# Kernel tuning notes

Hardware: AMD Instinct MI355X
Metric: run time of the kernel (lower is better)

## Reference

```python
import jax, jax.numpy as jnp
import numpy as np

HIDDEN = 2048
N_HEADS = 32
N_KV_HEADS = 8
HEAD_DIM = HIDDEN // N_HEADS  # 64
KV_GROUPS = N_HEADS // N_KV_HEADS  # 4
ROPE_THETA = 10000.0
BSZ, SEQ = 2, 2048


def setup_inputs() -> dict:
    key = jax.random.key(0)
    ks = jax.random.split(key, 5)
    s = 0.02
    hidden_states = jax.random.normal(ks[0], (BSZ, SEQ, HIDDEN), jnp.float32)
    position_ids = jnp.broadcast_to(jnp.arange(SEQ, dtype=jnp.int32), (BSZ, SEQ))
    Wq = jax.random.normal(ks[1], (HIDDEN, HIDDEN), jnp.float32) * s
    Wk = jax.random.normal(ks[2], (N_KV_HEADS * HEAD_DIM, HIDDEN), jnp.float32) * s
    Wv = jax.random.normal(ks[3], (N_KV_HEADS * HEAD_DIM, HIDDEN), jnp.float32) * s
    Wo = jax.random.normal(ks[4], (HIDDEN, HIDDEN), jnp.float32) * s
    return {"hidden_states": hidden_states, "position_ids": position_ids,
            "Wq": Wq, "Wk": Wk, "Wv": Wv, "Wo": Wo}


def _rope_cos_sin(position_ids):
    # Llama rotary embedding: inv_freq over even dims, emb = [freqs, freqs]
    inv_freq = 1.0 / (ROPE_THETA ** (jnp.arange(0, HEAD_DIM, 2, dtype=jnp.float32) / HEAD_DIM))  # [Hd/2]
    freqs = position_ids.astype(jnp.float32)[..., None] * inv_freq  # [B, S, Hd/2]
    emb = jnp.concatenate([freqs, freqs], axis=-1)  # [B, S, Hd]
    return jnp.cos(emb), jnp.sin(emb)


def _rotate_half(x):
    x1, x2 = jnp.split(x, 2, axis=-1)
    return jnp.concatenate([-x2, x1], axis=-1)


def reference(hidden_states, position_ids, Wq, Wk, Wv, Wo):
    bsz, seq_len, _ = hidden_states.shape
    # projections (nn.Linear: y = x @ W.T)
    q = (hidden_states @ Wq.T).reshape(bsz, seq_len, N_HEADS, HEAD_DIM).transpose(0, 2, 1, 3)
    k = (hidden_states @ Wk.T).reshape(bsz, seq_len, N_KV_HEADS, HEAD_DIM).transpose(0, 2, 1, 3)
    v = (hidden_states @ Wv.T).reshape(bsz, seq_len, N_KV_HEADS, HEAD_DIM).transpose(0, 2, 1, 3)
    cos, sin = _rope_cos_sin(position_ids)  # [B, S, Hd]
    cos = cos[:, None, :, :]
    sin = sin[:, None, :, :]
    q = q * cos + _rotate_half(q) * sin
    k = k * cos + _rotate_half(k) * sin
    # GQA expand kv heads to full head count
    k = jnp.repeat(k, KV_GROUPS, axis=1)  # [B, H, S, Hd]
    v = jnp.repeat(v, KV_GROUPS, axis=1)
    # naive full-softmax attention (no causal mask, matching the source)
    scores = jnp.einsum('bhqd,bhkd->bhqk', q, k) / jnp.sqrt(jnp.float32(HEAD_DIM))
    attn_w = jax.nn.softmax(scores, axis=-1)
    attn_o = jnp.einsum('bhqk,bhkd->bhqd', attn_w, v)
    attn_o = attn_o.transpose(0, 2, 1, 3).reshape(bsz, seq_len, HIDDEN)
    return attn_o @ Wo.T
```

## Files before the change

kernel.cpp:

```cpp
#include <hip/hip_runtime.h>
#include <hip/hip_bf16.h>
#include <stdint.h>

#define HID 2048
#define NH 32
#define NKV 8
#define HD 64
#define BSZ 2
#define SEQ 2048
#define NROWS (BSZ*SEQ)
#define KVCOLS (NKV*HD)
#define QKVN 3072

typedef __attribute__((ext_vector_type(8))) short bf16x8;
typedef __attribute__((ext_vector_type(4))) float f32x4;
typedef __attribute__((ext_vector_type(16))) float f32x16;
typedef __attribute__((ext_vector_type(2))) unsigned int u32x2;

__device__ __forceinline__ unsigned short f2bf(float f) {
  union { float f; uint32_t u; } v; v.f = f;
  uint32_t r = v.u + 0x7FFFu + ((v.u >> 16) & 1u);
  return (unsigned short)(r >> 16);
}

__device__ __forceinline__ unsigned pack_bf16(float a, float b) {
  union { __hip_bfloat162 h; unsigned u; } cv;
  cv.h = __float22bfloat162_rn(make_float2(a, b));
  return cv.u;
}

__device__ __forceinline__ float sum16(const f32x16& s) {
  float a0 = s[0] + s[1], a1 = s[2] + s[3], a2 = s[4] + s[5], a3 = s[6] + s[7];
  float a4 = s[8] + s[9], a5 = s[10] + s[11], a6 = s[12] + s[13], a7 = s[14] + s[15];
  float b0 = a0 + a1, b1 = a2 + a3, b2 = a4 + a5, b3 = a6 + a7;
  return (b0 + b1) + (b2 + b3);
}

#define MKPB(S, B0) ({ \
  unsigned A_ = pack_bf16((S)[B0], (S)[(B0)+1]); \
  unsigned C_ = pack_bf16((S)[(B0)+2], (S)[(B0)+3]); \
  unsigned B_ = pack_bf16((S)[(B0)+4], (S)[(B0)+5]); \
  unsigned D_ = pack_bf16((S)[(B0)+6], (S)[(B0)+7]); \
  u32x2 r0_ = __builtin_amdgcn_permlane32_swap(A_, B_, false, false); \
  u32x2 r1_ = __builtin_amdgcn_permlane32_swap(C_, D_, false, false); \
  union { uint4 u; bf16x8 v; } cv_; \
  cv_.u.x = r0_.x; cv_.u.y = r1_.x; cv_.u.z = r0_.y; cv_.u.w = r1_.y; \
  cv_.v; })

#define ROPE_C (-0.41524101186092029f)
#define QSCL 0.18033688011112042f

#define C0 2097152
#define C1 3145728
#define C2 3407872
#define C3 3670016
#define CT 4718592
__global__ __launch_bounds__(256) void cvt_all(
    const float* __restrict__ hs, const float* __restrict__ wq,
    const float* __restrict__ wk, const float* __restrict__ wv,
    const float* __restrict__ wo,
    unsigned short* __restrict__ xb, unsigned short* __restrict__ wqkv,
    unsigned short* __restrict__ wob) {
  int i4 = blockIdx.x * 256 + threadIdx.x;
  const int stride = gridDim.x * 256;
  for (; i4 < CT; i4 += stride) {
    const float* src; unsigned short* dst;
    if (i4 < C0)      { src = hs + (size_t)i4 * 4;            dst = xb   + (size_t)i4 * 4; }
    else if (i4 < C1) { src = wq + (size_t)(i4 - C0) * 4;     dst = wqkv + (size_t)(i4 - C0) * 4; }
    else if (i4 < C2) { src = wk + (size_t)(i4 - C1) * 4;     dst = wqkv + 4194304 + (size_t)(i4 - C1) * 4; }
    else if (i4 < C3) { src = wv + (size_t)(i4 - C2) * 4;     dst = wqkv + 5242880 + (size_t)(i4 - C2) * 4; }
    else              { src = wo + (size_t)(i4 - C3) * 4;     dst = wob  + (size_t)(i4 - C3) * 4; }
    float4 v = *(const float4*)src;
    ushort4 o;
    o.x = f2bf(v.x); o.y = f2bf(v.y); o.z = f2bf(v.z); o.w = f2bf(v.w);
    *(ushort4*)dst = o;
  }
}

#define BM 128
#define BN 128
#define BK 32

__global__ __launch_bounds__(256) void gemm_btn(
    const unsigned short* __restrict__ A,
    const unsigned short* __restrict__ B,
    float* __restrict__ C,
    int M, int N, int K)
{
  __shared__ unsigned short As[2][BM * BK];
  __shared__ unsigned short Bs[2][BN * BK];
  const int t = threadIdx.x;
  const int w = t >> 6, l = t & 63;
  const int wr = w >> 1, wc = w & 1;

  const int nwg = gridDim.x * gridDim.y;
  const int lin = blockIdx.y * gridDim.x + blockIdx.x;
  const int swz = (lin & 7) * (nwg >> 3) + (lin >> 3);
  const int bx = swz % gridDim.x, by = swz / gridDim.x;

  const int row0 = by * BM, col0 = bx * BN;
  const int lr = l & 15, lk = (l >> 4) * 8;

  f32x4 acc[4][4];
  for (int i = 0; i < 4; ++i)
    for (int j = 0; j < 4; ++j)
      acc[i][j] = (f32x4){0.f, 0.f, 0.f, 0.f};

  auto stage = [&](int bi, int k0) {
    #pragma unroll
    for (int i = 0; i < 2; ++i) {
      int ebase = i * 2048 + w * 512;
      int e = ebase + l * 8;
      const unsigned short* srcA = A + (size_t)(row0 + (e >> 5)) * K + k0 + (e & 31);
      const unsigned short* srcB = B + (size_t)(col0 + (e >> 5)) * K + k0 + (e & 31);
      __builtin_amdgcn_global_load_lds((const __attribute__((address_space(1))) void*)srcA,
          (__attribute__((address_space(3))) void*)&As[bi][ebase], 16, 0, 0);
      __builtin_amdgcn_global_load_lds((const __attribute__((address_space(1))) void*)srcB,
          (__attribute__((address_space(3))) void*)&Bs[bi][ebase], 16, 0, 0);
    }
  };

  stage(0, 0);
  __syncthreads();
  int bi = 0;
  for (int k0 = 0; k0 < K; k0 += BK) {
    if (k0 + BK < K) stage(bi ^ 1, k0 + BK);
    bf16x8 a[4], b[4];
    #pragma unroll
    for (int mi = 0; mi < 4; ++mi)
      a[mi] = *(const bf16x8*)&As[bi][(wr * 64 + mi * 16 + lr) * BK + lk];
    #pragma unroll
    for (int ni = 0; ni < 4; ++ni)
      b[ni] = *(const bf16x8*)&Bs[bi][(wc * 64 + ni * 16 + lr) * BK + lk];
    #pragma unroll
    for (int mi = 0; mi < 4; ++mi)
      #pragma unroll
      for (int ni = 0; ni < 4; ++ni)
        acc[mi][ni] = __builtin_amdgcn_mfma_f32_16x16x32_bf16(a[mi], b[ni], acc[mi][ni], 0, 0, 0);
    __syncthreads();
    bi ^= 1;
  }

  const int crow = (l >> 4) * 4, ccol = l & 15;
  #pragma unroll
  for (int mi = 0; mi < 4; ++mi)
    #pragma unroll
    for (int ni = 0; ni < 4; ++ni) {
      float* cp = C + (size_t)(row0 + wr * 64 + mi * 16 + crow) * N + col0 + wc * 64 + ni * 16 + ccol;
      #pragma unroll
      for (int r = 0; r < 4; ++r)
        cp[(size_t)r * N] = acc[mi][ni][r];
    }
}

__global__ __launch_bounds__(256) void gemm_qkv(
    const unsigned short* __restrict__ A,
    const unsigned short* __restrict__ B,
    const int* __restrict__ pos_ids,
    unsigned short* __restrict__ Qb,
    unsigned short* __restrict__ Kb,
    unsigned short* __restrict__ Vt)
{
  __shared__ unsigned short Sh[4 * BM * BK];
  unsigned short* As = Sh;
  unsigned short* Bs = Sh + 2 * BM * BK;
  const int t = threadIdx.x;
  const int w = t >> 6, l = t & 63;
  const int wr = w >> 1, wc = w & 1;

  const int nwg = gridDim.x * gridDim.y;
  const int lin = blockIdx.y * gridDim.x + blockIdx.x;
  const int swz = (lin & 7) * (nwg >> 3) + (lin >> 3);
  const int bx = swz % gridDim.x, by = swz / gridDim.x;

  const int row0 = by * BM, col0 = bx * BN;
  const int lr = l & 15, lk = (l >> 4) * 8;

  f32x4 acc[4][4];
  for (int i = 0; i < 4; ++i)
    for (int j = 0; j < 4; ++j)
      acc[i][j] = (f32x4){0.f, 0.f, 0.f, 0.f};

  auto stage = [&](int bi, int k0) {
    #pragma unroll
    for (int i = 0; i < 2; ++i) {
      int ebase = i * 2048 + w * 512;
      int e = ebase + l * 8;
      const unsigned short* srcA = A + (size_t)(row0 + (e >> 5)) * HID + k0 + (e & 31);
      const unsigned short* srcB = B + (size_t)(col0 + (e >> 5)) * HID + k0 + (e & 31);
      __builtin_amdgcn_global_load_lds((const __attribute__((address_space(1))) void*)srcA,
          (__attribute__((address_space(3))) void*)&As[bi * BM * BK + ebase], 16, 0, 0);
      __builtin_amdgcn_global_load_lds((const __attribute__((address_space(1))) void*)srcB,
          (__attribute__((address_space(3))) void*)&Bs[bi * BN * BK + ebase], 16, 0, 0);
    }
  };

  stage(0, 0);
  __syncthreads();
  int bi = 0;
  for (int k0 = 0; k0 < HID; k0 += BK) {
    if (k0 + BK < HID) stage(bi ^ 1, k0 + BK);
    bf16x8 a[4], b[4];
    #pragma unroll
    for (int mi = 0; mi < 4; ++mi)
      a[mi] = *(const bf16x8*)&As[bi * BM * BK + (wr * 64 + mi * 16 + lr) * BK + lk];
    #pragma unroll
    for (int ni = 0; ni < 4; ++ni)
      b[ni] = *(const bf16x8*)&Bs[bi * BN * BK + (wc * 64 + ni * 16 + lr) * BK + lk];
    #pragma unroll
    for (int mi = 0; mi < 4; ++mi)
      #pragma unroll
      for (int ni = 0; ni < 4; ++ni)
        acc[mi][ni] = __builtin_amdgcn_mfma_f32_16x16x32_bf16(a[mi], b[ni], acc[mi][ni], 0, 0, 0);
    __syncthreads();
    bi ^= 1;
  }

  const int crow = (l >> 4) * 4, ccol = l & 15;
  const int colbase = col0 + wc * 64;
  const int b = row0 >> 11;

  if (colbase < HID + KVCOLS) {
    const bool isQ = colbase < HID;
    const float scl = isQ ? QSCL : 1.0f;
    const int hh = (isQ ? colbase : colbase - HID) >> 6;
    unsigned short* base = (isQ ? Qb + ((size_t)(b * NH + hh) * SEQ) * HD
                                : Kb + ((size_t)(b * NKV + hh) * SEQ) * HD);
    const float invf0 = exp2f((float)ccol * ROPE_C);
    const float invf1 = exp2f((float)(ccol + 16) * ROPE_C);
    #pragma unroll
    for (int mi = 0; mi < 4; ++mi) {
      const int rowb = row0 + wr * 64 + mi * 16 + crow;
      #pragma unroll
      for (int r = 0; r < 4; ++r) {
        const int row = rowb + r;
        const int s = row & (SEQ - 1);
        const float pos = (float)pos_ids[row];
        #pragma unroll
        for (int ni = 0; ni < 2; ++ni) {
          float sn, cs;
          __sincosf(pos * (ni ? invf1 : invf0), &sn, &cs);
          const float x1 = acc[mi][ni][r], x2 = acc[mi][ni + 2][r];
          unsigned short* p = base + (size_t)s * HD + ni * 16 + ccol;
          p[0]  = f2bf((x1 * cs - x2 * sn) * scl);
          p[32] = f2bf((x2 * cs + x1 * sn) * scl);
        }
      }
    }
  } else {
    const int cv = colbase - (HID + KVCOLS);
    const int kh = cv >> 6;
    unsigned short* vbase = Vt + ((size_t)(b * NKV + kh) * HD) * SEQ;
    const int s0row = (row0 + wr * 64) & (SEQ - 1);
    char* Tw = (char*)Sh + w * 8192;
    #pragma unroll
    for (int ni = 0; ni < 4; ++ni) {
      const int d = ni * 16 + ccol;
      #pragma unroll
      for (int mi = 0; mi < 4; ++mi) {
        const int sl = mi * 16 + crow;
        ushort4 o;
        o.x = f2bf(acc[mi][ni][0]);
        o.y = f2bf(acc[mi][ni][1]);
        o.z = f2bf(acc[mi][ni][2]);
        o.w = f2bf(acc[mi][ni][3]);
        *(ushort4*)(Tw + ((d * 128 + sl * 2) ^ ((d & 7) << 4))) = o;
      }
    }
    asm volatile("s_waitcnt lgkmcnt(0)" ::: "memory");
    __builtin_amdgcn_sched_barrier(0);
    const int dl = l >> 3, sg = l & 7;
    #pragma unroll
    for (int dg = 0; dg < 8; ++dg) {
      const int d = dg * 8 + dl;
      uint4 v = *(const uint4*)(Tw + ((d * 128 + sg * 16) ^ ((d & 7) << 4)));
      *(uint4*)(vbase + (size_t)d * SEQ + s0row + sg * 8) = v;
    }
  }
}

__global__ __launch_bounds__(512, 4) void attn_kernel(
    const unsigned short* __restrict__ Qb,
    const unsigned short* __restrict__ Kb,
    const unsigned short* __restrict__ Vt,
    unsigned short* __restrict__ AO)
{
  __shared__ unsigned short Ks[2][64 * 64];
  __shared__ unsigned short Vs[2][64 * 64];

  const int lin = blockIdx.x;
  const int bid = (lin & 7) * 64 + (lin >> 3);
  const int qtile = bid & 7;
  const int h = (bid >> 3) & 31;
  const int b = bid >> 8;
  const int kh = h >> 2;
  const int t = threadIdx.x, w = t >> 6, l = t & 63;
  const int lq = l & 31, hi = l >> 5;
  const int sw = (lq & 7) << 4;
  const int qrow = qtile * 256 + w * 32 + lq;

  bf16x8 qf[4];
  {
    const unsigned short* Qrow = Qb + ((size_t)(b * NH + h) * SEQ + qrow) * HD;
    #pragma unroll
    for (int dk = 0; dk < 4; ++dk)
      qf[dk] = *(const bf16x8*)(Qrow + dk * 16 + hi * 8);
  }

  const unsigned short* Kt  = Kb + (size_t)(b * NKV + kh) * SEQ * HD;
  const unsigned short* Vth = Vt + (size_t)(b * NKV + kh) * HD * SEQ;

  const int dest = t * 16;
  const int srow = dest >> 7;
  const int scol = dest & 127;
  const int wdest = dest ^ ((srow & 7) << 4);
  const char* KsrcBase = (const char*)Kt + dest;
  const char* VsrcBase = (const char*)(Vth + (size_t)srow * SEQ) + scol;

  uint4 kreg, vreg;
  auto issue = [&](int kv0) {
    kreg = *(const uint4*)(KsrcBase + (size_t)kv0 * 128);
    vreg = *(const uint4*)(VsrcBase + kv0 * 2);
  };
  auto lwrite = [&](int si) {
    *(uint4*)((char*)Ks[si] + wdest) = kreg;
    *(uint4*)((char*)Vs[si] + wdest) = vreg;
  };

  const f32x16 Z = {0,0,0,0,0,0,0,0,0,0,0,0,0,0,0,0};
  float lsum = 0.f;
  f32x16 o0 = Z, o1 = Z;

  issue(0);
  lwrite(0);
  __syncthreads();

  int bi = 0;
  for (int it = 0; it < SEQ / 64; ++it) {
    const bool more = (it + 1 < SEQ / 64);
    if (more) issue((it + 1) * 64);

    const char* Kp = (const char*)Ks[bi];
    const char* Vp = (const char*)Vs[bi];

    f32x16 s0, s1;
    __builtin_amdgcn_s_setprio(1);
    {
      bf16x8 kf0 = *(const bf16x8*)(Kp + lq * 128 + ((hi * 16) ^ sw));
      bf16x8 kf1 = *(const bf16x8*)(Kp + 4096 + lq * 128 + ((hi * 16) ^ sw));
      s0 = __builtin_amdgcn_mfma_f32_32x32x16_bf16(kf0, qf[0], Z, 0, 0, 0);
      s1 = __builtin_amdgcn_mfma_f32_32x32x16_bf16(kf1, qf[0], Z, 0, 0, 0);
    }
    #pragma unroll
    for (int dk = 1; dk < 4; ++dk) {
      const int cb = dk * 32 + hi * 16;
      bf16x8 kf0 = *(const bf16x8*)(Kp + lq * 128 + (cb ^ sw));
      bf16x8 kf1 = *(const bf16x8*)(Kp + 4096 + lq * 128 + (cb ^ sw));
      s0 = __builtin_amdgcn_mfma_f32_32x32x16_bf16(kf0, qf[dk], s0, 0, 0, 0);
      s1 = __builtin_amdgcn_mfma_f32_32x32x16_bf16(kf1, qf[dk], s1, 0, 0, 0);
    }
    __builtin_amdgcn_s_setprio(0);

    #pragma unroll
    for (int r = 0; r < 16; ++r) { s0[r] = exp2f(s0[r]); s1[r] = exp2f(s1[r]); }
    float rs = sum16(s0) + sum16(s1);
    rs += __shfl_xor(rs, 32);
    lsum += rs;

    bf16x8 pb0 = MKPB(s0, 0), pb1 = MKPB(s0, 8), pb2 = MKPB(s1, 0), pb3 = MKPB(s1, 8);

    __builtin_amdgcn_s_setprio(1);
    #pragma unroll
    for (int ks = 0; ks < 4; ++ks) {
      const int cb = ks * 32 + hi * 16;
      bf16x8 vf0 = *(const bf16x8*)(Vp + lq * 128 + (cb ^ sw));
      bf16x8 vf1 = *(const bf16x8*)(Vp + 4096 + lq * 128 + (cb ^ sw));
      bf16x8 pa = (ks == 0) ? pb0 : (ks == 1) ? pb1 : (ks == 2) ? pb2 : pb3;
      o0 = __builtin_amdgcn_mfma_f32_32x32x16_bf16(vf0, pa, o0, 0, 0, 0);
      o1 = __builtin_amdgcn_mfma_f32_32x32x16_bf16(vf1, pa, o1, 0, 0, 0);
    }
    __builtin_amdgcn_s_setprio(0);

    if (more) lwrite(bi ^ 1);
    __syncthreads();
    bi ^= 1;
  }

  const float inv = 1.0f / lsum;
  unsigned short* op = AO + ((size_t)(b * SEQ) + qrow) * HID + h * 64;
  #pragma unroll
  for (int r = 0; r < 16; r += 2) {
    const int d = (r & 3) + 8 * (r >> 2) + 4 * hi;
    *(unsigned*)(op + d)      = pack_bf16(o0[r] * inv, o0[r + 1] * inv);
    *(unsigned*)(op + 32 + d) = pack_bf16(o1[r] * inv, o1[r + 1] * inv);
  }
}

extern "C" void kernel_launch(void* const* d_in, const int* in_sizes, int n_in,
                              void* d_out, int out_size, void* d_ws, size_t ws_size,
                              hipStream_t stream) {
  const float* hs  = (const float*)d_in[0];
  const int*   pos = (const int*)d_in[1];
  const float* Wq  = (const float*)d_in[2];
  const float* Wk  = (const float*)d_in[3];
  const float* Wv  = (const float*)d_in[4];
  const float* Wo  = (const float*)d_in[5];
  float* out = (float*)d_out;

  char* ws = (char*)d_ws;
  size_t off = 0;
  auto carve = [&](size_t bytes) { void* p = ws + off; off += (bytes + 255) & ~(size_t)255; return p; };

  unsigned short* Xb    = (unsigned short*)carve((size_t)NROWS * HID * 2);
  unsigned short* Wqkvb = (unsigned short*)carve((size_t)QKVN * HID * 2);
  unsigned short* Wob   = (unsigned short*)carve((size_t)HID * HID * 2);
  unsigned short* Qbh   = (unsigned short*)carve((size_t)NROWS * HID * 2);
  unsigned short* Kbh   = (unsigned short*)carve((size_t)NROWS * KVCOLS * 2);
  unsigned short* Vtb   = (unsigned short*)carve((size_t)NROWS * KVCOLS * 2);
  unsigned short* AO    = (unsigned short*)carve((size_t)NROWS * HID * 2);

  cvt_all<<<2048, 256, 0, stream>>>(hs, Wq, Wk, Wv, Wo, Xb, Wqkvb, Wob);

  gemm_qkv<<<dim3(QKVN / BN, NROWS / BM), 256, 0, stream>>>(Xb, Wqkvb, pos, Qbh, Kbh, Vtb);

  attn_kernel<<<BSZ * NH * (SEQ / 256), 512, 0, stream>>>(Qbh, Kbh, Vtb, AO);

  gemm_btn<<<dim3(HID / BN, NROWS / BM), 256, 0, stream>>>(AO, Wob, out, NROWS, HID, HID);
}
```

Baseline: 259.0 us.

## Compute softmax row sums via MFMA with ones; precompute RoPE cos/sin table

The attention kernel no longer sums exponentials with VALU adds and a cross-lane shuffle each tile. It adds a third MFMA per k-step that multiplies the bf16 probabilities by a ones vector, so the row sum accumulates on the matrix unit from the same rounded values that feed the PV product. Separately, the RoPE cos/sin values are computed once per row in the conversion kernel into a float2 table, and the QKV GEMM epilogue reads this table instead of calling sincos for every output. The trade-off is extra MFMA work in the attention inner loop and extra global traffic for the table in exchange for fewer VALU/transcendental ops.

```diff
diff --git a/kernel.cpp b/kernel.cpp
--- a/kernel.cpp
+++ b/kernel.cpp
@@ -27,13 +27,6 @@
   union { __hip_bfloat162 h; unsigned u; } cv;
   cv.h = __float22bfloat162_rn(make_float2(a, b));
   return cv.u;
-}
-
-__device__ __forceinline__ float sum16(const f32x16& s) {
-  float a0 = s[0] + s[1], a1 = s[2] + s[3], a2 = s[4] + s[5], a3 = s[6] + s[7];
-  float a4 = s[8] + s[9], a5 = s[10] + s[11], a6 = s[12] + s[13], a7 = s[14] + s[15];
-  float b0 = a0 + a1, b1 = a2 + a3, b2 = a4 + a5, b3 = a6 + a7;
-  return (b0 + b1) + (b2 + b3);
 }
 
 #define MKPB(S, B0) ({ \
@@ -55,15 +48,31 @@
 #define C2 3407872
 #define C3 3670016
 #define CT 4718592
+#define CT2 (CT + 32768)
 __global__ __launch_bounds__(256) void cvt_all(
     const float* __restrict__ hs, const float* __restrict__ wq,
     const float* __restrict__ wk, const float* __restrict__ wv,
-    const float* __restrict__ wo,
+    const float* __restrict__ wo, const int* __restrict__ pos_ids,
     unsigned short* __restrict__ xb, unsigned short* __restrict__ wqkv,
-    unsigned short* __restrict__ wob) {
+    unsigned short* __restrict__ wob, float2* __restrict__ tab) {
   int i4 = blockIdx.x * 256 + threadIdx.x;
   const int stride = gridDim.x * 256;
-  for (; i4 < CT; i4 += stride) {
+  for (; i4 < CT2; i4 += stride) {
+    if (i4 >= CT) {
+      const int idx = i4 - CT;
+      const int row = idx >> 3, jb = (idx & 7) * 4;
+      const float pos = (float)pos_ids[row];
+      float2 e[4];
+      #pragma unroll
+      for (int jj = 0; jj < 4; ++jj) {
+        float sn, cs;
+        __sincosf(pos * exp2f((float)(jb + jj) * ROPE_C), &sn, &cs);
+        e[jj].x = cs; e[jj].y = sn;
+      }
+      *(float4*)(tab + (size_t)row * 32 + jb)     = *(const float4*)&e[0];
+      *(float4*)(tab + (size_t)row * 32 + jb + 2) = *(const float4*)&e[2];
+      continue;
+    }
     const float* src; unsigned short* dst;
     if (i4 < C0)      { src = hs + (size_t)i4 * 4;            dst = xb   + (size_t)i4 * 4; }
     else if (i4 < C1) { src = wq + (size_t)(i4 - C0) * 4;     dst = wqkv + (size_t)(i4 - C0) * 4; }
@@ -156,7 +165,7 @@
 __global__ __launch_bounds__(256) void gemm_qkv(
     const unsigned short* __restrict__ A,
     const unsigned short* __restrict__ B,
-    const int* __restrict__ pos_ids,
+    const float2* __restrict__ tab,
     unsigned short* __restrict__ Qb,
     unsigned short* __restrict__ Kb,
     unsigned short* __restrict__ Vt)
@@ -226,8 +235,6 @@
     const int hh = (isQ ? colbase : colbase - HID) >> 6;
     unsigned short* base = (isQ ? Qb + ((size_t)(b * NH + hh) * SEQ) * HD
                                 : Kb + ((size_t)(b * NKV + hh) * SEQ) * HD);
-    const float invf0 = exp2f((float)ccol * ROPE_C);
-    const float invf1 = exp2f((float)(ccol + 16) * ROPE_C);
     #pragma unroll
     for (int mi = 0; mi < 4; ++mi) {
       const int rowb = row0 + wr * 64 + mi * 16 + crow;
@@ -235,15 +242,14 @@
       for (int r = 0; r < 4; ++r) {
         const int row = rowb + r;
         const int s = row & (SEQ - 1);
-        const float pos = (float)pos_ids[row];
+        const float2* tr = tab + (size_t)row * 32 + ccol;
         #pragma unroll
         for (int ni = 0; ni < 2; ++ni) {
-          float sn, cs;
-          __sincosf(pos * (ni ? invf1 : invf0), &sn, &cs);
+          const float2 cssn = tr[ni * 16];
           const float x1 = acc[mi][ni][r], x2 = acc[mi][ni + 2][r];
           unsigned short* p = base + (size_t)s * HD + ni * 16 + ccol;
-          p[0]  = f2bf((x1 * cs - x2 * sn) * scl);
-          p[32] = f2bf((x2 * cs + x1 * sn) * scl);
+          p[0]  = f2bf((x1 * cssn.x - x2 * cssn.y) * scl);
+          p[32] = f2bf((x2 * cssn.x + x1 * cssn.y) * scl);
         }
       }
     }
@@ -307,6 +313,14 @@
       qf[dk] = *(const bf16x8*)(Qrow + dk * 16 + hi * 8);
   }
 
+  bf16x8 ones;
+  {
+    union { bf16x8 v; unsigned short us[8]; } u;
+    #pragma unroll
+    for (int i = 0; i < 8; ++i) u.us[i] = 0x3F80;
+    ones = u.v;
+  }
+
   const unsigned short* Kt  = Kb + (size_t)(b * NKV + kh) * SEQ * HD;
   const unsigned short* Vth = Vt + (size_t)(b * NKV + kh) * HD * SEQ;
 
@@ -328,8 +342,7 @@
   };
 
   const f32x16 Z = {0,0,0,0,0,0,0,0,0,0,0,0,0,0,0,0};
-  float lsum = 0.f;
-  f32x16 o0 = Z, o1 = Z;
+  f32x16 o0 = Z, o1 = Z, osum = Z;
 
   issue(0);
   lwrite(0);
@@ -363,9 +376,6 @@
 
     #pragma unroll
     for (int r = 0; r < 16; ++r) { s0[r] = exp2f(s0[r]); s1[r] = exp2f(s1[r]); }
-    float rs = sum16(s0) + sum16(s1);
-    rs += __shfl_xor(rs, 32);
-    lsum += rs;
 
     bf16x8 pb0 = MKPB(s0, 0), pb1 = MKPB(s0, 8), pb2 = MKPB(s1, 0), pb3 = MKPB(s1, 8);
 
@@ -378,6 +388,7 @@
       bf16x8 pa = (ks == 0) ? pb0 : (ks == 1) ? pb1 : (ks == 2) ? pb2 : pb3;
       o0 = __builtin_amdgcn_mfma_f32_32x32x16_bf16(vf0, pa, o0, 0, 0, 0);
       o1 = __builtin_amdgcn_mfma_f32_32x32x16_bf16(vf1, pa, o1, 0, 0, 0);
+      osum = __builtin_amdgcn_mfma_f32_32x32x16_bf16(ones, pa, osum, 0, 0, 0);
     }
     __builtin_amdgcn_s_setprio(0);
 
@@ -386,7 +397,7 @@
     bi ^= 1;
   }
 
-  const float inv = 1.0f / lsum;
+  const float inv = 1.0f / osum[0];
   unsigned short* op = AO + ((size_t)(b * SEQ) + qrow) * HID + h * 64;
   #pragma unroll
   for (int r = 0; r < 16; r += 2) {
@@ -418,10 +429,11 @@
   unsigned short* Kbh   = (unsigned short*)carve((size_t)NROWS * KVCOLS * 2);
   unsigned short* Vtb   = (unsigned short*)carve((size_t)NROWS * KVCOLS * 2);
   unsigned short* AO    = (unsigned short*)carve((size_t)NROWS * HID * 2);
-
-  cvt_all<<<2048, 256, 0, stream>>>(hs, Wq, Wk, Wv, Wo, Xb, Wqkvb, Wob);
-
-  gemm_qkv<<<dim3(QKVN / BN, NROWS / BM), 256, 0, stream>>>(Xb, Wqkvb, pos, Qbh, Kbh, Vtb);
+  float2*         Tab   = (float2*)carve((size_t)NROWS * 32 * sizeof(float2));
+
+  cvt_all<<<2048, 256, 0, stream>>>(hs, Wq, Wk, Wv, Wo, pos, Xb, Wqkvb, Wob, Tab);
+
+  gemm_qkv<<<dim3(QKVN / BN, NROWS / BM), 256, 0, stream>>>(Xb, Wqkvb, Tab, Qbh, Kbh, Vtb);
 
   attn_kernel<<<BSZ * NH * (SEQ / 256), 512, 0, stream>>>(Qbh, Kbh, Vtb, AO);
 
```

Measured after the change: 260.8 us. No clear change (+0.7%).
